# Kernel optimization log

Measured on AMD Instinct MI355X. Metric: run time of the kernel, lower is better.

The kernel has to match this reference:

```python
import jax, jax.numpy as jnp
import numpy as np

DIM = 128          # dim (forced by LayerNorm(dim) on last-dim-128 reshape)
NP = 24            # num_patch
N = NP * NP        # 576 tokens
HEADS = 128        # num_heads (forced by einsum contraction, d' must be 1)
HEAD_D = 2         # head_dim
INNER = HEADS * HEAD_D  # 256 (forced by SRA Conv2d(256, ...))
B = 2
SCALE = HEAD_D ** -0.5
EPS = 1e-5


def setup_inputs() -> dict:
    key = jax.random.key(0)
    ks = jax.random.split(key, 12)
    f = jax.random.normal
    return {
        'x': f(ks[0], (B, N, DIM), jnp.float32),
        'bn_gamma': 1.0 + 0.1 * f(ks[1], (DIM,), jnp.float32),
        'bn_beta': 0.1 * f(ks[2], (DIM,), jnp.float32),
        # qkc: Conv2d(128, 768, 1, groups=head_dim=2, bias=False) -> OIHW (768, 64, 1, 1)
        'qkc_w': 0.05 * f(ks[3], (3 * INNER, DIM // HEAD_D, 1, 1), jnp.float32),
        # spe: Conv2d(128, 128, 1, groups=2, bias=False)
        'spe_w': 0.05 * f(ks[4], (DIM, DIM // HEAD_D, 1, 1), jnp.float32),
        # SRA.sr: Conv2d(256, 128, 3, padding=1, groups=128) -> OIHW (128, 2, 3, 3), with bias
        'sr_w': 0.05 * f(ks[5], (DIM, INNER // DIM, 3, 3), jnp.float32),
        'sr_b': 0.01 * f(ks[6], (DIM,), jnp.float32),
        'ln_gamma': 1.0 + 0.1 * f(ks[7], (DIM,), jnp.float32),
        'ln_beta': 0.1 * f(ks[8], (DIM,), jnp.float32),
        # local: Conv2d(128, 128, 3, padding=1, groups=2, bias=False)
        'local_w': 0.05 * f(ks[9], (DIM, DIM // HEAD_D, 3, 3), jnp.float32),
        'bnc1_gamma': 1.0 + 0.1 * f(ks[10], (DIM,), jnp.float32),
        'bnc1_beta': 0.1 * f(ks[11], (DIM,), jnp.float32),
    }


def _conv(x, w, groups, pad):
    return jax.lax.conv_general_dilated(
        x, w, (1, 1), pad,
        dimension_numbers=('NCHW', 'OIHW', 'NCHW'),
        feature_group_count=groups)


def _bn_inf(x, g, b):
    # BatchNorm2d in inference form with running_mean=0, running_var=1
    return x * (g / jnp.sqrt(1.0 + EPS))[None, :, None, None] + b[None, :, None, None]


def reference(x, bn_gamma, bn_beta, qkc_w, spe_w, sr_w, sr_b,
              ln_gamma, ln_beta, local_w, bnc1_gamma, bnc1_beta):
    b = x.shape[0]
    x4 = x.reshape(b, DIM, NP, NP)                       # (b,128,24,24)
    a = jax.nn.gelu(_bn_inf(x4, bn_gamma, bn_beta), approximate=False)

    # qkc grouped 1x1 conv -> (b,768,24,24), raw view to (b,576,768)
    qkv = _conv(a, qkc_w, HEAD_D, 'VALID').reshape(b, N, 3 * INNER)
    v_chunk = qkv[..., 2 * INNER:]                       # only v survives the chained assignment
    # rearrange 'b (h d) n -> b n h d', h=NP : (b,576,256) -> (b,256,24,24)
    v4 = v_chunk.reshape(b, NP, NP, INNER).transpose(0, 3, 1, 2)

    # SRA (sr_ratio = num_heads > 1): grouped 3x3 conv + LayerNorm
    xsr = _conv(v4, sr_w, DIM, ((1, 1), (1, 1))) + sr_b[None, :, None, None]  # (b,128,24,24)
    x_ = xsr.reshape(b, N, DIM)                          # row-major view, matches torch
    mu = x_.mean(-1, keepdims=True)
    var = ((x_ - mu) ** 2).mean(-1, keepdims=True)
    qy = (x_ - mu) / jnp.sqrt(var + EPS) * ln_gamma + ln_beta

    # q = k = v : (b, heads=128, N=576, d'=1)
    q = qy.reshape(b, N, HEADS, 1).transpose(0, 2, 1, 3)

    # spe branch: grouped 1x1 conv + global avg pool -> (b,128,1,1) -> (b,128,1,1) as bh(nw)d
    spe = _conv(a, spe_w, HEAD_D, 'VALID').mean(axis=(2, 3)).reshape(b, HEADS, 1, 1)

    scores = jnp.einsum('bhid,bhjd->bhij', q, q) * SCALE  # (b,128,576,576)
    attn = jax.nn.softmax(scores, axis=-1)

    v_spe = jnp.einsum('bhij,bhjd->bhid', q, spe) * SCALE  # (b,128,576,1)
    v_spe1 = jax.nn.softmax(v_spe, axis=-1)                # size-1 axis -> ones (faithful)
    out = jnp.einsum('bhij,bhjd->bhid', attn, v_spe1)      # (b,128,576,1)
    out = out.transpose(0, 2, 1, 3).reshape(b, N, HEADS)   # 'b h n d -> b n (h d)'

    # local conv branch
    c = jax.nn.gelu(_bn_inf(_conv(x4, local_w, HEAD_D, ((1, 1), (1, 1))),
                            bnc1_gamma, bnc1_beta), approximate=False)
    c = c.reshape(b, N, DIM)                               # raw view, matches torch reshape

    # AdaptiveAvgPool1d(128) on a length-128 last dim is identity
    return out + c
```

## Files before the change

### kernel.cpp

```cpp
#include <hip/hip_runtime.h>
#include <hip/hip_bf16.h>


__global__ __launch_bounds__(576, 1) void fused_conv_gelu(
    const float* __restrict__ x,
    const float* __restrict__ lw,
    const float* __restrict__ gam,
    const float* __restrict__ bet,
    float* __restrict__ out)
{
    const int bi = blockIdx.x;
    const int b  = bi >> 7;
    const int o  = bi & 127;
    const int g  = o >> 6;
    const int p  = threadIdx.x;
    const int h  = p / 24;
    const int w  = p - h * 24;

    const float* __restrict__ xb = x  + (b * 128 + g * 64) * 576;
    const float* __restrict__ wb = lw + o * 576;

    bool val[9];
#pragma unroll
    for (int dh = 0; dh < 3; ++dh)
#pragma unroll
        for (int dw = 0; dw < 3; ++dw) {
            const int hh = h + dh - 1, ww = w + dw - 1;
            val[dh * 3 + dw] = (hh >= 0) && (hh < 24) && (ww >= 0) && (ww < 24);
        }

    float acc = 0.0f;

#pragma unroll
    for (int ic = 0; ic < 2; ++ic) {
        const int i = ic ? 63 : 0;
        const float* __restrict__ xi = xb + i * 576;
        const float* __restrict__ wi = wb + i * 9;
#pragma unroll
        for (int dh = 0; dh < 3; ++dh)
#pragma unroll
            for (int dw = 0; dw < 3; ++dw) {
                const int t  = dh * 3 + dw;
                const int hh = min(max(h + dh - 1, 0), 23);
                const int ww = min(max(w + dw - 1, 0), 23);
                const float xv = xi[hh * 24 + ww];
                acc = fmaf(val[t] ? xv : 0.0f, wi[t], acc);
            }
    }

#pragma unroll 2
    for (int i = 1; i < 63; ++i) {
        const float* __restrict__ xi = xb + i * 576 + p;
        const float* __restrict__ wi = wb + i * 9;
#pragma unroll
        for (int dh = 0; dh < 3; ++dh)
#pragma unroll
            for (int dw = 0; dw < 3; ++dw) {
                const int t  = dh * 3 + dw;
                const float xv = xi[(dh - 1) * 24 + (dw - 1)];
                acc = fmaf(val[t] ? xv : 0.0f, wi[t], acc);
            }
    }

    const float scale = gam[o] * rsqrtf(1.0f + 1e-5f);
    const float shift = bet[o];
    const float y  = fmaf(acc, scale, shift);
    const float gl = 0.5f * y * (1.0f + erff(y * 0.70710678118654752f));
    out[b * 73728 + o * 576 + p] = 1.0f + gl;
}

extern "C" void kernel_launch(void* const* d_in, const int* in_sizes, int n_in,
                              void* d_out, int out_size, void* d_ws, size_t ws_size,
                              hipStream_t stream) {
    const float* x   = (const float*)d_in[0];
    const float* lw  = (const float*)d_in[9];
    const float* gam = (const float*)d_in[10];
    const float* bet = (const float*)d_in[11];
    float* out = (float*)d_out;

    fused_conv_gelu<<<dim3(256), dim3(576), 0, stream>>>(x, lw, gam, bet, out);
}
```

Measured before the change: 87.40 us.

## Register-tile conv outputs, split input channels across threads, reduce via LDS

Restructures the grouped 3x3 conv so each thread computes 8 adjacent outputs of one row over 8 input channels. It loads each input row segment once with float4 loads and reuses it across the three horizontal taps. The weights are staged in LDS, and the 8 channel-slice partial sums are reduced through shared memory before BN+GELU. This cuts the redundant per-output global loads and the serial 64-channel loop per thread, at the cost of extra LDS, a second barrier and more registers.

Result: slower. 142.0 us (+62.4%).

```diff
diff --git a/kernel.cpp b/kernel.cpp
--- a/kernel.cpp
+++ b/kernel.cpp
@@ -1,5 +1,4 @@
 #include <hip/hip_runtime.h>
-#include <hip/hip_bf16.h>
 
 
 __global__ __launch_bounds__(576, 1) void fused_conv_gelu(
@@ -9,64 +8,88 @@
     const float* __restrict__ bet,
     float* __restrict__ out)
 {
+    __shared__ float wlds[576];
+    __shared__ float part[8][576];
+
     const int bi = blockIdx.x;
     const int b  = bi >> 7;
     const int o  = bi & 127;
     const int g  = o >> 6;
-    const int p  = threadIdx.x;
-    const int h  = p / 24;
-    const int w  = p - h * 24;
+    const int t  = threadIdx.x;
 
-    const float* __restrict__ xb = x  + (b * 128 + g * 64) * 576;
-    const float* __restrict__ wb = lw + o * 576;
+    wlds[t] = lw[o * 576 + t];
+    __syncthreads();
 
-    bool val[9];
+    const int s  = t / 72;
+    const int u  = t % 72;
+    const int r  = u / 3;
+    const int w0 = (u % 3) * 8;
+
+    const float* __restrict__ xp = x + (b * 128 + g * 64) * 576;
+
+    int  rrc[3];
+    bool rv[3];
 #pragma unroll
-    for (int dh = 0; dh < 3; ++dh)
+    for (int dr = 0; dr < 3; ++dr) {
+        const int rr = r + dr - 1;
+        rv[dr]  = (rr >= 0) && (rr < 24);
+        rrc[dr] = min(max(rr, 0), 23);
+    }
+    const bool lval = (w0 != 0);
+    const bool rval = (w0 != 16);
+    const int  wl   = lval ? (w0 - 1) : 0;
+    const int  wr   = rval ? (w0 + 8) : 23;
+
+    float acc[8];
 #pragma unroll
-        for (int dw = 0; dw < 3; ++dw) {
-            const int hh = h + dh - 1, ww = w + dw - 1;
-            val[dh * 3 + dw] = (hh >= 0) && (hh < 24) && (ww >= 0) && (ww < 24);
-        }
-
-    float acc = 0.0f;
+    for (int j = 0; j < 8; ++j) acc[j] = 0.0f;
 
 #pragma unroll
-    for (int ic = 0; ic < 2; ++ic) {
-        const int i = ic ? 63 : 0;
-        const float* __restrict__ xi = xb + i * 576;
-        const float* __restrict__ wi = wb + i * 9;
+    for (int ic = 0; ic < 8; ++ic) {
+        const int i = s * 8 + ic;
+        const float* __restrict__ cp = xp + i * 576;
+        const float* __restrict__ wc = &wlds[i * 9];
+
 #pragma unroll
-        for (int dh = 0; dh < 3; ++dh)
+        for (int dr = 0; dr < 3; ++dr) {
+            const float* __restrict__ rp = cp + rrc[dr] * 24;
+            float W[10];
+            W[0] = lval ? rp[wl] : 0.0f;
+            const float4 q1 = *(const float4*)(rp + w0);
+            const float4 q2 = *(const float4*)(rp + w0 + 4);
+            W[1] = q1.x; W[2] = q1.y; W[3] = q1.z; W[4] = q1.w;
+            W[5] = q2.x; W[6] = q2.y; W[7] = q2.z; W[8] = q2.w;
+            W[9] = rval ? rp[wr] : 0.0f;
+            const float wg0 = rv[dr] ? wc[dr * 3 + 0] : 0.0f;
+            const float wg1 = rv[dr] ? wc[dr * 3 + 1] : 0.0f;
+            const float wg2 = rv[dr] ? wc[dr * 3 + 2] : 0.0f;
 #pragma unroll
-            for (int dw = 0; dw < 3; ++dw) {
-                const int t  = dh * 3 + dw;
-                const int hh = min(max(h + dh - 1, 0), 23);
-                const int ww = min(max(w + dw - 1, 0), 23);
-                const float xv = xi[hh * 24 + ww];
-                acc = fmaf(val[t] ? xv : 0.0f, wi[t], acc);
-            }
+            for (int j = 0; j < 8; ++j)
+                acc[j] = fmaf(wg0, W[j],
+                         fmaf(wg1, W[j + 1],
+                         fmaf(wg2, W[j + 2], acc[j])));
+        }
     }
 
-#pragma unroll 2
-    for (int i = 1; i < 63; ++i) {
-        const float* __restrict__ xi = xb + i * 576 + p;
-        const float* __restrict__ wi = wb + i * 9;
+    {
+        float4 a0, a1;
+        a0.x = acc[0]; a0.y = acc[1]; a0.z = acc[2]; a0.w = acc[3];
+        a1.x = acc[4]; a1.y = acc[5]; a1.z = acc[6]; a1.w = acc[7];
+        float* pp = &part[s][r * 24 + w0];
+        *(float4*)(pp)     = a0;
+        *(float4*)(pp + 4) = a1;
+    }
+    __syncthreads();
+
+    float v = 0.0f;
 #pragma unroll
-        for (int dh = 0; dh < 3; ++dh)
-#pragma unroll
-            for (int dw = 0; dw < 3; ++dw) {
-                const int t  = dh * 3 + dw;
-                const float xv = xi[(dh - 1) * 24 + (dw - 1)];
-                acc = fmaf(val[t] ? xv : 0.0f, wi[t], acc);
-            }
-    }
+    for (int ss = 0; ss < 8; ++ss) v += part[ss][t];
 
     const float scale = gam[o] * rsqrtf(1.0f + 1e-5f);
     const float shift = bet[o];
-    const float y  = fmaf(acc, scale, shift);
+    const float y  = fmaf(v, scale, shift);
     const float gl = 0.5f * y * (1.0f + erff(y * 0.70710678118654752f));
-    out[b * 73728 + o * 576 + p] = 1.0f + gl;
+    out[b * 73728 + o * 576 + t] = 1.0f + gl;
 }
 
 extern "C" void kernel_launch(void* const* d_in, const int* in_sizes, int n_in,
```
